# Kernel tuning notes

Hardware: AMD Instinct MI355X
Metric: run time of the kernel (lower is better)

Reference implementation:

```python
import jax, jax.numpy as jnp
import numpy as np

N_NODES = 1_000_000
N_EDGES = 10_000_000
HIDDEN = 8
N_GRAPHS = 64


def _gcn_conv(h_in, W, b, src, dst, deg_inv_sqrt, n_nodes):
    """One PyG GCNConv: symmetric-normalized aggregation over (A + I)."""
    h = h_in @ W  # [N, out]
    norm = deg_inv_sqrt[src] * deg_inv_sqrt[dst]  # [E]
    msgs = h[src] * norm[:, None]  # gather + scale, [E, out]
    out = jax.ops.segment_sum(msgs, dst, num_segments=n_nodes)  # scatter-add
    out = out + h * (deg_inv_sqrt * deg_inv_sqrt)[:, None]  # self-loop term
    return out + b


def setup_inputs() -> dict:
    key = jax.random.key(0)
    ks = jax.random.split(key, 12)
    x = jax.random.uniform(ks[0], (N_NODES, 1), dtype=jnp.float32)
    edge_index = jax.random.randint(ks[1], (2, N_EDGES), 0, N_NODES, dtype=jnp.int64)
    indices = jax.random.randint(ks[2], (N_GRAPHS,), 0, N_NODES, dtype=jnp.int64)
    # Glorot-ish init for GCNConv linear layers (no bias in lin; GCNConv bias separate)
    W1 = jax.random.normal(ks[3], (1, HIDDEN), dtype=jnp.float32) * (1.0 / np.sqrt(1))
    W2 = jax.random.normal(ks[4], (HIDDEN, HIDDEN), dtype=jnp.float32) * (1.0 / np.sqrt(HIDDEN))
    W3 = jax.random.normal(ks[5], (HIDDEN, HIDDEN), dtype=jnp.float32) * (1.0 / np.sqrt(HIDDEN))
    W4 = jax.random.normal(ks[6], (HIDDEN, HIDDEN), dtype=jnp.float32) * (1.0 / np.sqrt(HIDDEN))
    b1 = jnp.zeros((HIDDEN,), jnp.float32)
    b2 = jnp.zeros((HIDDEN,), jnp.float32)
    b3 = jnp.zeros((HIDDEN,), jnp.float32)
    b4 = jnp.zeros((HIDDEN,), jnp.float32)
    return {"x": x, "edge_index": edge_index, "indices": indices,
            "W1": W1, "b1": b1, "W2": W2, "b2": b2,
            "W3": W3, "b3": b3, "W4": W4, "b4": b4}


def reference(x, edge_index, indices, W1, b1, W2, b2, W3, b3, W4, b4):
    n_nodes = x.shape[0]
    src, dst = edge_index[0], edge_index[1]
    # degree under A + I (symmetric GCN normalization)
    deg = jax.ops.segment_sum(jnp.ones_like(dst, dtype=x.dtype), dst,
                              num_segments=n_nodes) + 1.0
    deg_inv_sqrt = jax.lax.rsqrt(deg)
    h = x
    for W, b, last in ((W1, b1, False), (W2, b2, False), (W3, b3, False), (W4, b4, True)):
        h = _gcn_conv(h, W, b, src, dst, deg_inv_sqrt, n_nodes)
        if not last:
            h = jax.nn.relu(h)
    return h[indices]  # one node embedding per batched graph, [B, 8]
```

## Files before the change

kernel.cpp:

```cpp
#include <hip/hip_runtime.h>
#include <hip/hip_fp16.h>

#define TPB 256
#define STPB 512
#define BTPB 512
#define NBK 256
#define BNODES 4096
#define QNODES 1024
#define CH 6144
#define CAPB 45056
#define QSTG 12288
#define CAP_L 262144

typedef unsigned int uv4 __attribute__((ext_vector_type(4)));
union H8 { uv4 u; __half2 h2[4]; };

__global__ __launch_bounds__(STPB) void scatter_sort(const int* __restrict__ dst,
                                                     const int* __restrict__ src,
                                                     int* __restrict__ tails,
                                                     unsigned* __restrict__ bdata, int nE) {
    __shared__ unsigned      stage[CH];
    __shared__ unsigned char bkt[CH];
    __shared__ int cnt[NBK], sstart[NBK], cur[NBK], cbase[NBK];
    __shared__ int wsum[STPB / 64];
    int t = threadIdx.x;
    long base = (long)blockIdx.x * CH;
    int m = (int)(((long)nE - base < CH) ? (nE - base) : CH);
    if (t < NBK) cnt[t] = 0;
    __syncthreads();
    for (int k = t * 4; k < m; k += STPB * 4) {
        if (k + 3 < m) {
            int4 d4 = *(const int4*)(dst + base + k);
            atomicAdd(&cnt[d4.x >> 12], 1);
            atomicAdd(&cnt[d4.y >> 12], 1);
            atomicAdd(&cnt[d4.z >> 12], 1);
            atomicAdd(&cnt[d4.w >> 12], 1);
        } else {
            int ke = (k + 4 < m) ? (k + 4) : m;
            for (int kk = k; kk < ke; ++kk)
                atomicAdd(&cnt[dst[base + kk] >> 12], 1);
        }
    }
    __syncthreads();
    int v = 0, incl = 0;
    if (t < NBK) {
        v = cnt[t]; incl = v;
#pragma unroll
        for (int o = 1; o < 64; o <<= 1) {
            int u = __shfl_up(incl, o, 64);
            if ((t & 63) >= o) incl += u;
        }
        if ((t & 63) == 63) wsum[t >> 6] = incl;
    }
    __syncthreads();
    if (t < NBK) {
        int wadd = 0;
#pragma unroll
        for (int w = 0; w < 3; ++w) wadd += (w < (t >> 6)) ? wsum[w] : 0;
        int ex = incl - v + wadd;
        sstart[t] = ex;
        cur[t] = ex;
        cbase[t] = v ? (t * CAPB + atomicAdd(&tails[t], v)) : 0;
    }
    __syncthreads();
    for (int k = t * 4; k < m; k += STPB * 4) {
        if (k + 3 < m) {
            int4 d4 = *(const int4*)(dst + base + k);
            int4 s4 = *(const int4*)(src + base + k);
            { int b = d4.x >> 12; int pos = atomicAdd(&cur[b], 1);
              stage[pos] = ((unsigned)(d4.x & 4095) << 20) | (unsigned)s4.x; bkt[pos] = (unsigned char)b; }
            { int b = d4.y >> 12; int pos = atomicAdd(&cur[b], 1);
              stage[pos] = ((unsigned)(d4.y & 4095) << 20) | (unsigned)s4.y; bkt[pos] = (unsigned char)b; }
            { int b = d4.z >> 12; int pos = atomicAdd(&cur[b], 1);
              stage[pos] = ((unsigned)(d4.z & 4095) << 20) | (unsigned)s4.z; bkt[pos] = (unsigned char)b; }
            { int b = d4.w >> 12; int pos = atomicAdd(&cur[b], 1);
              stage[pos] = ((unsigned)(d4.w & 4095) << 20) | (unsigned)s4.w; bkt[pos] = (unsigned char)b; }
        } else {
            int ke = (k + 4 < m) ? (k + 4) : m;
            for (int kk = k; kk < ke; ++kk) {
                int d = dst[base + kk], s = src[base + kk];
                int b = d >> 12; int pos = atomicAdd(&cur[b], 1);
                stage[pos] = ((unsigned)(d & 4095) << 20) | (unsigned)s; bkt[pos] = (unsigned char)b;
            }
        }
    }
    __syncthreads();
    for (int k = t; k < m; k += STPB) {
        int b = bkt[k];
        bdata[cbase[b] + (k - sstart[b])] = stage[k];
    }
}

__global__ __launch_bounds__(BTPB) void quarter_csr(const unsigned* __restrict__ bdata,
                                                    const int* __restrict__ tails,
                                                    const float* __restrict__ x,
                                                    const float* __restrict__ W1,
                                                    int* __restrict__ rowptr,
                                                    __half* __restrict__ hs,
                                                    int* __restrict__ col, int n, int NB) {
    __shared__ int      off[QNODES];
    __shared__ int      wsum[BTPB / 64];
    __shared__ int      wredQ[BTPB / 64];
    __shared__ int      wredP[BTPB / 64];
    __shared__ int      sQb, sTot, sPb;
    __shared__ unsigned stg[QSTG];
    int bid = blockIdx.x, t = threadIdx.x;
    int xcd = bid & 7, slot = bid >> 3;
    int b = (slot >> 2) * 8 + xcd;
    int q = slot & 3;
    if (b >= NB) return;
    int e0 = b * CAPB, e1 = e0 + tails[b];
    for (int j = t; j < QNODES; j += BTPB) off[j] = 0;
    int partial = (t < b) ? tails[t] : 0;
#pragma unroll
    for (int o = 32; o > 0; o >>= 1) partial += __shfl_down(partial, o, 64);
    if ((t & 63) == 0) wredP[t >> 6] = partial;
    __syncthreads();
    if (t == 0) {
        int s = 0;
#pragma unroll
        for (int w = 0; w < BTPB / 64; ++w) s += wredP[w];
        sPb = s;
    }
    int before = 0;
    for (int k = e0 + t * 4; k < e1; k += BTPB * 4) {
        if (k + 3 < e1) {
            uv4 p4 = *(const uv4*)(bdata + k);
#pragma unroll
            for (int z = 0; z < 4; ++z) {
                int j = (int)(p4[z] >> 20); int jq = j >> 10;
                if (jq == q) atomicAdd(&off[j & 1023], 1);
                before += (jq < q) ? 1 : 0;
            }
        } else {
            for (int kk = k; kk < e1; ++kk) {
                int j = (int)(bdata[kk] >> 20); int jq = j >> 10;
                if (jq == q) atomicAdd(&off[j & 1023], 1);
                before += (jq < q) ? 1 : 0;
            }
        }
    }
#pragma unroll
    for (int o = 32; o > 0; o >>= 1) before += __shfl_down(before, o, 64);
    if ((t & 63) == 0) wredQ[t >> 6] = before;
    __syncthreads();
    if (t == 0) {
        int s = 0;
#pragma unroll
        for (int w = 0; w < BTPB / 64; ++w) s += wredQ[w];
        sQb = s;
    }
    int a = off[2 * t], c = off[2 * t + 1];
    int s2 = a + c;
    int incl = s2;
#pragma unroll
    for (int o = 1; o < 64; o <<= 1) {
        int u = __shfl_up(incl, o, 64);
        if ((t & 63) >= o) incl += u;
    }
    if ((t & 63) == 63) wsum[t >> 6] = incl;
    __syncthreads();
    int wadd = 0;
#pragma unroll
    for (int w = 0; w < BTPB / 64 - 1; ++w) wadd += (w < (t >> 6)) ? wsum[w] : 0;
    int pex = incl - s2 + wadd;
    off[2 * t]     = pex;
    off[2 * t + 1] = pex + a;
    if (t == BTPB - 1) sTot = pex + s2;
    int PbQb = sPb + sQb;
    {
        int node0 = (b << 12) + (q << 10) + 2 * t;
        float4 w0 = ((const float4*)W1)[0];
        float4 w1 = ((const float4*)W1)[1];
        if (node0 + 1 < n) {
            int2 rp; rp.x = PbQb + pex; rp.y = PbQb + pex + a;
            *(int2*)(rowptr + node0) = rp;
            float2 xv = *(const float2*)(x + node0);
            float dv0 = rsqrtf((float)a + 1.0f);
            float dv1 = rsqrtf((float)c + 1.0f);
            float xd0 = xv.x * dv0, xd1 = xv.y * dv1;
            H8 o0, o1;
            o0.h2[0] = __floats2half2_rn(xd0 * w0.x, xd0 * w0.y);
            o0.h2[1] = __floats2half2_rn(xd0 * w0.z, xd0 * w0.w);
            o0.h2[2] = __floats2half2_rn(xd0 * w1.x, xd0 * w1.y);
            o0.h2[3] = __floats2half2_rn(xd0 * w1.z, xd0 * w1.w);
            o1.h2[0] = __floats2half2_rn(xd1 * w0.x, xd1 * w0.y);
            o1.h2[1] = __floats2half2_rn(xd1 * w0.z, xd1 * w0.w);
            o1.h2[2] = __floats2half2_rn(xd1 * w1.x, xd1 * w1.y);
            o1.h2[3] = __floats2half2_rn(xd1 * w1.z, xd1 * w1.w);
            ((uv4*)hs)[node0]     = o0.u;
            ((uv4*)hs)[node0 + 1] = o1.u;
        } else {
            if (node0 <= n)     rowptr[node0]     = PbQb + pex;
            if (node0 + 1 <= n) rowptr[node0 + 1] = PbQb + pex + a;
            if (node0 < n) {
                float dv = rsqrtf((float)a + 1.0f);
                float xd = x[node0] * dv;
                H8 o;
                o.h2[0] = __floats2half2_rn(xd * w0.x, xd * w0.y);
                o.h2[1] = __floats2half2_rn(xd * w0.z, xd * w0.w);
                o.h2[2] = __floats2half2_rn(xd * w1.x, xd * w1.y);
                o.h2[3] = __floats2half2_rn(xd * w1.z, xd * w1.w);
                ((uv4*)hs)[node0] = o.u;
            }
        }
    }
    __syncthreads();
    for (int k = e0 + t * 4; k < e1; k += BTPB * 4) {
        if (k + 3 < e1) {
            uv4 p4 = *(const uv4*)(bdata + k);
#pragma unroll
            for (int z = 0; z < 4; ++z) {
                int j = (int)(p4[z] >> 20);
                if ((j >> 10) == q) {
                    int pos = atomicAdd(&off[j & 1023], 1);
                    stg[pos] = p4[z] & 0xFFFFFu;
                }
            }
        } else {
            for (int kk = k; kk < e1; ++kk) {
                unsigned p = bdata[kk];
                int j = (int)(p >> 20);
                if ((j >> 10) == q) {
                    int pos = atomicAdd(&off[j & 1023], 1);
                    stg[pos] = p & 0xFFFFFu;
                }
            }
        }
    }
    __syncthreads();
    int tot = sTot;
    for (int k = t; k < tot; k += BTPB)
        col[PbQb + k] = (int)stg[k];
}

__global__ void seed_mark_q(const int* __restrict__ idx, int B, int* __restrict__ mark,
                            int* __restrict__ L, int* __restrict__ qq) {
    int t = threadIdx.x;
    if (t < B) {
        int u = idx[t];
        if (atomicCAS(&mark[u], 0, 1) == 0)
            L[atomicAdd(&qq[7], 1)] = u;
    }
}

__global__ __launch_bounds__(TPB) void expand_f(int* __restrict__ L, int* __restrict__ qq,
                                                int tier,
                                                const int* __restrict__ rowptr,
                                                const int* __restrict__ col,
                                                int* __restrict__ mark) {
    int hi = qq[7];
    int stride = gridDim.x * blockDim.x;
    int lane = threadIdx.x & 63;
    for (int r = blockIdx.x * blockDim.x + threadIdx.x; r < hi; r += stride) {
        int u = L[r];
        if (mark[u] != tier - 1) continue;
        int e0 = rowptr[u], e1 = rowptr[u + 1];
        for (int k = e0; k < e1; ++k) {
            int s = col[k];
            bool ok = (mark[s] == 0) && (atomicCAS(&mark[s], 0, tier) == 0);
            unsigned long long msk = __ballot(ok);
            if (msk) {
                int leader = __builtin_ctzll(msk);
                int cntw = __builtin_popcountll(msk);
                int basep = 0;
                if (lane == leader) basep = atomicAdd(&qq[7], cntw);
                basep = __shfl(basep, leader, 64);
                if (ok) {
                    int myoff = __builtin_popcountll(msk & ((1ull << lane) - 1ull));
                    L[basep + myoff] = s;
                }
            }
        }
    }
}

__global__ void pull_tier(const int* __restrict__ L, const int* __restrict__ qq,
                          int tagMax, const int* __restrict__ mark,
                          const int* __restrict__ rowptr, const int* __restrict__ col,
                          const __half* __restrict__ hs_in, const float* __restrict__ bias,
                          const float* __restrict__ W, __half* __restrict__ hs_out) {
    int r = blockIdx.x * blockDim.x + threadIdx.x;
    if (r >= qq[7]) return;
    int u = L[r];
    if (mark[u] > tagMax) return;
    const uv4* hv = (const uv4*)hs_in;
    H8 p; p.u = hv[u];
    float2 a0 = __half22float2(p.h2[0]);
    float2 a1 = __half22float2(p.h2[1]);
    float2 a2 = __half22float2(p.h2[2]);
    float2 a3 = __half22float2(p.h2[3]);
    int s = rowptr[u], e = rowptr[u + 1];
    for (int k = s; k < e; ++k) {
        H8 q; q.u = hv[col[k]];
        float2 b0 = __half22float2(q.h2[0]);
        float2 b1 = __half22float2(q.h2[1]);
        float2 b2 = __half22float2(q.h2[2]);
        float2 b3 = __half22float2(q.h2[3]);
        a0.x += b0.x; a0.y += b0.y; a1.x += b1.x; a1.y += b1.y;
        a2.x += b2.x; a2.y += b2.y; a3.x += b3.x; a3.y += b3.y;
    }
    float d = rsqrtf((float)(e - s) + 1.0f);
    float t[8] = {a0.x * d, a0.y * d, a1.x * d, a1.y * d,
                  a2.x * d, a2.y * d, a3.x * d, a3.y * d};
#pragma unroll
    for (int k = 0; k < 8; ++k) {
        float v = t[k] + bias[k];
        t[k] = v > 0.0f ? v : 0.0f;
    }
    float h[8];
#pragma unroll
    for (int j = 0; j < 8; ++j) {
        float acc = 0.0f;
#pragma unroll
        for (int k = 0; k < 8; ++k) acc += t[k] * W[k * 8 + j];
        h[j] = acc * d;
    }
    H8 o;
    o.h2[0] = __floats2half2_rn(h[0], h[1]);
    o.h2[1] = __floats2half2_rn(h[2], h[3]);
    o.h2[2] = __floats2half2_rn(h[4], h[5]);
    o.h2[3] = __floats2half2_rn(h[6], h[7]);
    ((uv4*)hs_out)[u] = o.u;
}

__global__ void pull_final(const int* __restrict__ idx, int B,
                           const int* __restrict__ rowptr, const int* __restrict__ col,
                           const __half* __restrict__ hs_in,
                           const float* __restrict__ b4, float* __restrict__ out) {
    int t = blockIdx.x * blockDim.x + threadIdx.x;
    if (t >= B) return;
    int u = idx[t];
    const uv4* hv = (const uv4*)hs_in;
    H8 p; p.u = hv[u];
    float2 a0 = __half22float2(p.h2[0]);
    float2 a1 = __half22float2(p.h2[1]);
    float2 a2 = __half22float2(p.h2[2]);
    float2 a3 = __half22float2(p.h2[3]);
    int s = rowptr[u], e = rowptr[u + 1];
    for (int k = s; k < e; ++k) {
        H8 q; q.u = hv[col[k]];
        float2 b0 = __half22float2(q.h2[0]);
        float2 b1 = __half22float2(q.h2[1]);
        float2 b2 = __half22float2(q.h2[2]);
        float2 b3 = __half22float2(q.h2[3]);
        a0.x += b0.x; a0.y += b0.y; a1.x += b1.x; a1.y += b1.y;
        a2.x += b2.x; a2.y += b2.y; a3.x += b3.x; a3.y += b3.y;
    }
    float d = rsqrtf((float)(e - s) + 1.0f);
    float* op = out + (size_t)t * 8;
    op[0] = a0.x * d + b4[0]; op[1] = a0.y * d + b4[1];
    op[2] = a1.x * d + b4[2]; op[3] = a1.y * d + b4[3];
    op[4] = a2.x * d + b4[4]; op[5] = a2.y * d + b4[5];
    op[6] = a3.x * d + b4[6]; op[7] = a3.y * d + b4[7];
}

extern "C" void kernel_launch(void* const* d_in, const int* in_sizes, int n_in,
                              void* d_out, int out_size, void* d_ws, size_t ws_size,
                              hipStream_t stream) {
    const float* x   = (const float*)d_in[0];
    const int*   ei  = (const int*)d_in[1];
    const int*   idx = (const int*)d_in[2];
    const float* W1  = (const float*)d_in[3];
    const float* b1  = (const float*)d_in[4];
    const float* W2  = (const float*)d_in[5];
    const float* b2  = (const float*)d_in[6];
    const float* W3  = (const float*)d_in[7];
    const float* b3  = (const float*)d_in[8];
    const float* W4  = (const float*)d_in[9];
    const float* b4  = (const float*)d_in[10];

    const int n = in_sizes[0];
    const int E = in_sizes[1] / 2;
    const int B = in_sizes[2];

    const int* src = ei;
    const int* dst = ei + E;

    const int NB = (n + BNODES - 1) / BNODES;

    size_t o_mark = 0;
    size_t o_rp   = o_mark + (size_t)n;
    size_t o_hsA  = o_rp   + (size_t)n + 8;
    size_t o_L    = o_hsA  + (size_t)n * 4;
    size_t o_col  = o_L    + CAP_L;
    size_t o_bd   = o_col  + (size_t)E;
    size_t o_sm   = o_bd   + (size_t)NB * CAPB;

    int*      mark   = (int*)d_ws + o_mark;
    int*      rowptr = (int*)d_ws + o_rp;
    __half*   hsA    = (__half*)((int*)d_ws + o_hsA);
    int*      L      = (int*)d_ws + o_L;
    int*      col    = (int*)d_ws + o_col;
    unsigned* bdata  = (unsigned*)((int*)d_ws + o_bd);
    __half*   hsB    = (__half*)bdata;
    int*      tails  = (int*)d_ws + o_sm;
    int*      qq     = tails + NBK;

    const int gs  = (int)(((long)E + CH - 1) / CH);
    const int nb2 = CAP_L / TPB;
    const int gq  = ((NB + 7) / 8) * 32;

    (void)hipMemsetAsync(mark, 0, (size_t)n * sizeof(int), stream);
    (void)hipMemsetAsync(tails, 0, (NBK + 16) * sizeof(int), stream);

    scatter_sort<<<gs, STPB, 0, stream>>>(dst, src, tails, bdata, E);

    quarter_csr<<<gq, BTPB, 0, stream>>>(bdata, tails, x, W1, rowptr, hsA, col, n, NB);

    seed_mark_q<<<1, 64, 0, stream>>>(idx, B, mark, L, qq);
    expand_f<<<64, TPB, 0, stream>>>(L, qq, 2, rowptr, col, mark);
    expand_f<<<128, TPB, 0, stream>>>(L, qq, 3, rowptr, col, mark);
    expand_f<<<256, TPB, 0, stream>>>(L, qq, 4, rowptr, col, mark);

    pull_tier<<<nb2, TPB, 0, stream>>>(L, qq, 4, mark, rowptr, col, hsA, b1, W2, hsB);
    pull_tier<<<nb2, TPB, 0, stream>>>(L, qq, 3, mark, rowptr, col, hsB, b2, W3, hsA);
    pull_tier<<<nb2, TPB, 0, stream>>>(L, qq, 2, mark, rowptr, col, hsA, b3, W4, hsB);
    pull_final<<<1, 64, 0, stream>>>(idx, B, rowptr, col, hsB, b4, (float*)d_out);
}
```

Measured before the change: 410.6 us.

## Fuse cone expansion and tier pulls into one cooperative persistent kernel

Replaces the eight small launches (seed, three frontier expansions, three tier pulls, final pull) with a single cooperative kernel that uses grid-wide syncs between phases. The aim is to remove per-launch overhead and idle gaps between tiny dependent kernels, which dominate once the work cone is small. In exchange it fixes the grid at 512x512 threads, so per-phase parallelism is bounded and grid.sync has its own cost. The old multi-launch path is kept as a fallback if the cooperative launch fails.

```diff
diff --git a/kernel.cpp b/kernel.cpp
--- a/kernel.cpp
+++ b/kernel.cpp
@@ -1,9 +1,14 @@
 #include <hip/hip_runtime.h>
 #include <hip/hip_fp16.h>
+#include <hip/hip_cooperative_groups.h>
+
+namespace cg = cooperative_groups;
 
 #define TPB 256
 #define STPB 512
 #define BTPB 512
+#define CPTB 512
+#define CGRID 512
 #define NBK 256
 #define BNODES 4096
 #define QNODES 1024
@@ -234,6 +239,141 @@
         col[PbQb + k] = (int)stg[k];
 }
 
+__device__ __forceinline__ void pull_rows(int gid, int gstride, int nrows, int tagMax,
+                                          const int* __restrict__ L,
+                                          const int* __restrict__ mark,
+                                          const int* __restrict__ rowptr,
+                                          const int* __restrict__ col,
+                                          const __half* __restrict__ hs_in,
+                                          const float* __restrict__ bias,
+                                          const float* __restrict__ W,
+                                          __half* __restrict__ hs_out) {
+    const uv4* hv = (const uv4*)hs_in;
+    for (int r = gid; r < nrows; r += gstride) {
+        int u = L[r];
+        if (mark[u] > tagMax) continue;
+        H8 p; p.u = hv[u];
+        float2 a0 = __half22float2(p.h2[0]);
+        float2 a1 = __half22float2(p.h2[1]);
+        float2 a2 = __half22float2(p.h2[2]);
+        float2 a3 = __half22float2(p.h2[3]);
+        int s = rowptr[u], e = rowptr[u + 1];
+        for (int k = s; k < e; ++k) {
+            H8 q; q.u = hv[col[k]];
+            float2 b0 = __half22float2(q.h2[0]);
+            float2 b1 = __half22float2(q.h2[1]);
+            float2 b2 = __half22float2(q.h2[2]);
+            float2 b3 = __half22float2(q.h2[3]);
+            a0.x += b0.x; a0.y += b0.y; a1.x += b1.x; a1.y += b1.y;
+            a2.x += b2.x; a2.y += b2.y; a3.x += b3.x; a3.y += b3.y;
+        }
+        float d = rsqrtf((float)(e - s) + 1.0f);
+        float t[8] = {a0.x * d, a0.y * d, a1.x * d, a1.y * d,
+                      a2.x * d, a2.y * d, a3.x * d, a3.y * d};
+#pragma unroll
+        for (int k = 0; k < 8; ++k) {
+            float v = t[k] + bias[k];
+            t[k] = v > 0.0f ? v : 0.0f;
+        }
+        float h[8];
+#pragma unroll
+        for (int j = 0; j < 8; ++j) {
+            float acc = 0.0f;
+#pragma unroll
+            for (int k = 0; k < 8; ++k) acc += t[k] * W[k * 8 + j];
+            h[j] = acc * d;
+        }
+        H8 o;
+        o.h2[0] = __floats2half2_rn(h[0], h[1]);
+        o.h2[1] = __floats2half2_rn(h[2], h[3]);
+        o.h2[2] = __floats2half2_rn(h[4], h[5]);
+        o.h2[3] = __floats2half2_rn(h[6], h[7]);
+        ((uv4*)hs_out)[u] = o.u;
+    }
+}
+
+__global__ __launch_bounds__(CPTB) void cone_pipeline(
+        const int* __restrict__ idx, int B,
+        int* __restrict__ mark, int* __restrict__ L, int* __restrict__ qq,
+        const int* __restrict__ rowptr, const int* __restrict__ col,
+        __half* __restrict__ hsA, __half* __restrict__ hsB,
+        const float* __restrict__ b1, const float* __restrict__ W2,
+        const float* __restrict__ b2, const float* __restrict__ W3,
+        const float* __restrict__ b3, const float* __restrict__ W4,
+        const float* __restrict__ b4, float* __restrict__ out) {
+    cg::grid_group g = cg::this_grid();
+    int gid = blockIdx.x * blockDim.x + threadIdx.x;
+    int gstride = gridDim.x * blockDim.x;
+    int lane = threadIdx.x & 63;
+
+    if (gid < B) {
+        int u = idx[gid];
+        if (atomicCAS(&mark[u], 0, 1) == 0)
+            L[atomicAdd(&qq[7], 1)] = u;
+    }
+    g.sync();
+
+    for (int tier = 2; tier <= 4; ++tier) {
+        int hi = qq[7];
+        for (int r = gid; r < hi; r += gstride) {
+            int u = L[r];
+            if (mark[u] != tier - 1) continue;
+            int e0 = rowptr[u], e1 = rowptr[u + 1];
+            for (int k = e0; k < e1; ++k) {
+                int s = col[k];
+                bool ok = (mark[s] == 0) && (atomicCAS(&mark[s], 0, tier) == 0);
+                unsigned long long msk = __ballot(ok);
+                if (msk) {
+                    int leader = __builtin_ctzll(msk);
+                    int cntw = __builtin_popcountll(msk);
+                    int basep = 0;
+                    if (lane == leader) basep = atomicAdd(&qq[7], cntw);
+                    basep = __shfl(basep, leader, 64);
+                    if (ok) {
+                        int myoff = __builtin_popcountll(msk & ((1ull << lane) - 1ull));
+                        L[basep + myoff] = s;
+                    }
+                }
+            }
+        }
+        g.sync();
+    }
+
+    int nrows = qq[7];
+    pull_rows(gid, gstride, nrows, 4, L, mark, rowptr, col, hsA, b1, W2, hsB);
+    g.sync();
+    pull_rows(gid, gstride, nrows, 3, L, mark, rowptr, col, hsB, b2, W3, hsA);
+    g.sync();
+    pull_rows(gid, gstride, nrows, 2, L, mark, rowptr, col, hsA, b3, W4, hsB);
+    g.sync();
+
+    if (gid < B) {
+        int u = idx[gid];
+        const uv4* hv = (const uv4*)hsB;
+        H8 p; p.u = hv[u];
+        float2 a0 = __half22float2(p.h2[0]);
+        float2 a1 = __half22float2(p.h2[1]);
+        float2 a2 = __half22float2(p.h2[2]);
+        float2 a3 = __half22float2(p.h2[3]);
+        int s = rowptr[u], e = rowptr[u + 1];
+        for (int k = s; k < e; ++k) {
+            H8 q; q.u = hv[col[k]];
+            float2 b0 = __half22float2(q.h2[0]);
+            float2 b1v = __half22float2(q.h2[1]);
+            float2 b2v = __half22float2(q.h2[2]);
+            float2 b3v = __half22float2(q.h2[3]);
+            a0.x += b0.x; a0.y += b0.y; a1.x += b1v.x; a1.y += b1v.y;
+            a2.x += b2v.x; a2.y += b2v.y; a3.x += b3v.x; a3.y += b3v.y;
+        }
+        float d = rsqrtf((float)(e - s) + 1.0f);
+        float* op = out + (size_t)gid * 8;
+        op[0] = a0.x * d + b4[0]; op[1] = a0.y * d + b4[1];
+        op[2] = a1.x * d + b4[2]; op[3] = a1.y * d + b4[3];
+        op[4] = a2.x * d + b4[4]; op[5] = a2.y * d + b4[5];
+        op[6] = a3.x * d + b4[6]; op[7] = a3.y * d + b4[7];
+    }
+}
+
 __global__ void seed_mark_q(const int* __restrict__ idx, int B, int* __restrict__ mark,
                             int* __restrict__ L, int* __restrict__ qq) {
     int t = threadIdx.x;
@@ -282,46 +422,7 @@
                           const float* __restrict__ W, __half* __restrict__ hs_out) {
     int r = blockIdx.x * blockDim.x + threadIdx.x;
     if (r >= qq[7]) return;
-    int u = L[r];
-    if (mark[u] > tagMax) return;
-    const uv4* hv = (const uv4*)hs_in;
-    H8 p; p.u = hv[u];
-    float2 a0 = __half22float2(p.h2[0]);
-    float2 a1 = __half22float2(p.h2[1]);
-    float2 a2 = __half22float2(p.h2[2]);
-    float2 a3 = __half22float2(p.h2[3]);
-    int s = rowptr[u], e = rowptr[u + 1];
-    for (int k = s; k < e; ++k) {
-        H8 q; q.u = hv[col[k]];
-        float2 b0 = __half22float2(q.h2[0]);
-        float2 b1 = __half22float2(q.h2[1]);
-        float2 b2 = __half22float2(q.h2[2]);
-        float2 b3 = __half22float2(q.h2[3]);
-        a0.x += b0.x; a0.y += b0.y; a1.x += b1.x; a1.y += b1.y;
-        a2.x += b2.x; a2.y += b2.y; a3.x += b3.x; a3.y += b3.y;
-    }
-    float d = rsqrtf((float)(e - s) + 1.0f);
-    float t[8] = {a0.x * d, a0.y * d, a1.x * d, a1.y * d,
-                  a2.x * d, a2.y * d, a3.x * d, a3.y * d};
-#pragma unroll
-    for (int k = 0; k < 8; ++k) {
-        float v = t[k] + bias[k];
-        t[k] = v > 0.0f ? v : 0.0f;
-    }
-    float h[8];
-#pragma unroll
-    for (int j = 0; j < 8; ++j) {
-        float acc = 0.0f;
-#pragma unroll
-        for (int k = 0; k < 8; ++k) acc += t[k] * W[k * 8 + j];
-        h[j] = acc * d;
-    }
-    H8 o;
-    o.h2[0] = __floats2half2_rn(h[0], h[1]);
-    o.h2[1] = __floats2half2_rn(h[2], h[3]);
-    o.h2[2] = __floats2half2_rn(h[4], h[5]);
-    o.h2[3] = __floats2half2_rn(h[6], h[7]);
-    ((uv4*)hs_out)[u] = o.u;
+    pull_rows(r, 1 << 30, r + 1, tagMax, L, mark, rowptr, col, hs_in, bias, W, hs_out);
 }
 
 __global__ void pull_final(const int* __restrict__ idx, int B,
@@ -408,13 +509,26 @@
 
     quarter_csr<<<gq, BTPB, 0, stream>>>(bdata, tails, x, W1, rowptr, hsA, col, n, NB);
 
-    seed_mark_q<<<1, 64, 0, stream>>>(idx, B, mark, L, qq);
-    expand_f<<<64, TPB, 0, stream>>>(L, qq, 2, rowptr, col, mark);
-    expand_f<<<128, TPB, 0, stream>>>(L, qq, 3, rowptr, col, mark);
-    expand_f<<<256, TPB, 0, stream>>>(L, qq, 4, rowptr, col, mark);
-
-    pull_tier<<<nb2, TPB, 0, stream>>>(L, qq, 4, mark, rowptr, col, hsA, b1, W2, hsB);
-    pull_tier<<<nb2, TPB, 0, stream>>>(L, qq, 3, mark, rowptr, col, hsB, b2, W3, hsA);
-    pull_tier<<<nb2, TPB, 0, stream>>>(L, qq, 2, mark, rowptr, col, hsA, b3, W4, hsB);
-    pull_final<<<1, 64, 0, stream>>>(idx, B, rowptr, col, hsB, b4, (float*)d_out);
-}
+    {
+        float* outp = (float*)d_out;
+        void* args[] = {
+            (void*)&idx, (void*)&B, (void*)&mark, (void*)&L, (void*)&qq,
+            (void*)&rowptr, (void*)&col, (void*)&hsA, (void*)&hsB,
+            (void*)&b1, (void*)&W2, (void*)&b2, (void*)&W3,
+            (void*)&b3, (void*)&W4, (void*)&b4, (void*)&outp
+        };
+        hipError_t err = hipLaunchCooperativeKernel((const void*)cone_pipeline,
+                                                    dim3(CGRID), dim3(CPTB),
+                                                    args, 0, stream);
+        if (err != hipSuccess) {
+            seed_mark_q<<<1, 64, 0, stream>>>(idx, B, mark, L, qq);
+            expand_f<<<64, TPB, 0, stream>>>(L, qq, 2, rowptr, col, mark);
+            expand_f<<<128, TPB, 0, stream>>>(L, qq, 3, rowptr, col, mark);
+            expand_f<<<256, TPB, 0, stream>>>(L, qq, 4, rowptr, col, mark);
+            pull_tier<<<nb2, TPB, 0, stream>>>(L, qq, 4, mark, rowptr, col, hsA, b1, W2, hsB);
+            pull_tier<<<nb2, TPB, 0, stream>>>(L, qq, 3, mark, rowptr, col, hsB, b2, W3, hsA);
+            pull_tier<<<nb2, TPB, 0, stream>>>(L, qq, 2, mark, rowptr, col, hsA, b3, W4, hsB);
+            pull_final<<<1, 64, 0, stream>>>(idx, B, rowptr, col, hsB, b4, (float*)d_out);
+        }
+    }
+}
```

Result: slower. 793.1 us (+93.2%).
